# Performance work log

Measured on AMD Instinct MI355X. Metric: run time of the kernel, lower is better.

## Reference

```python
import jax, jax.numpy as jnp
import numpy as np

HALFKP = 64 * 5 * 64          # 20480
PAD = HALFKP                  # padding row index
L1, L2, L3 = 256, 31, 32
NB = 8                        # layer-stack / psqt buckets
EMB_DIM = L1 + NB             # 264


def setup_inputs() -> dict:
    key = jax.random.key(0)
    ks = jax.random.split(key, 16)
    B = 16384
    w_idx = jax.random.randint(ks[0], (B, 32), 0, HALFKP + 1)
    b_idx = jax.random.randint(ks[1], (B, 32), 0, HALFKP + 1)
    us = jax.random.uniform(ks[2], (B,), dtype=jnp.float32)
    them = jax.random.uniform(ks[3], (B,), dtype=jnp.float32)
    piece_count = jax.random.randint(ks[4], (B,), 2, 33)
    sigma = 0.025
    emb = jax.random.uniform(ks[5], (HALFKP + 1, EMB_DIM), jnp.float32, -sigma, sigma)
    emb = emb.at[PAD].set(0.0)
    def lin(k, out_f, in_f):
        bound = 1.0 / np.sqrt(in_f)
        k1, k2 = jax.random.split(k)
        W = jax.random.uniform(k1, (out_f, in_f), jnp.float32, -bound, bound)
        b = jax.random.uniform(k2, (out_f,), jnp.float32, -bound, bound)
        return W, b
    # StackedLinear init: replicate slot-0 weights across all buckets
    w1_0, b1_0 = lin(ks[6], L2 + 1, L1)
    w1 = jnp.tile(w1_0, (NB, 1)); b1 = jnp.tile(b1_0, NB)
    fw1 = jnp.zeros((L2 + 1, L1), jnp.float32)
    fb1 = jnp.zeros((L2 + 1,), jnp.float32)
    w2_0, b2_0 = lin(ks[7], L3, L2 * 2)
    w2 = jnp.tile(w2_0, (NB, 1)); b2 = jnp.tile(b2_0, NB)
    wo_0, _ = lin(ks[8], 1, L3)
    wo = jnp.tile(wo_0, (NB, 1)); bo = jnp.zeros((NB,), jnp.float32)
    return {"emb": emb, "w1": w1, "b1": b1, "fw1": fw1, "fb1": fb1,
            "w2": w2, "b2": b2, "wo": wo, "bo": bo,
            "us": us, "them": them,
            "w_idx": w_idx, "b_idx": b_idx, "piece_count": piece_count}


def reference(emb, w1, b1, fw1, fb1, w2, b2, wo, bo, us, them,
              w_idx, b_idx, piece_count):
    emb_eff = emb.at[PAD].set(0.0)                      # padding row contributes 0
    wp = emb_eff[w_idx].sum(axis=1)                     # [B, 264]
    bp = emb_eff[b_idx].sum(axis=1)
    w, wpsqt = wp[:, :L1], wp[:, L1:]
    b, bpsqt = bp[:, :L1], bp[:, L1:]
    us_c = us[:, None]; them_c = them[:, None]
    l0 = us_c * jnp.concatenate([w, b], 1) + them_c * jnp.concatenate([b, w], 1)
    l0 = jnp.clip(l0, 0.0, 1.0)                         # [B, 512]
    h = L1 // 2
    l0 = jnp.concatenate([l0[:, :h] * l0[:, h:2*h],
                          l0[:, 2*h:3*h] * l0[:, 3*h:]], 1) * (127.0 / 128.0)  # [B,256]
    bucket = jnp.clip((piece_count - 1) // 4, 0, 7)     # [B]
    # l1: factorized stacked linear, gather the bucket's slice only
    W1 = (w1 + jnp.tile(fw1, (NB, 1))).reshape(NB, L2 + 1, L1)
    B1 = (b1 + jnp.tile(fb1, NB)).reshape(NB, L2 + 1)
    l1c = jnp.einsum('bi,bji->bj', l0, W1[bucket]) + B1[bucket]   # [B,32]
    l1x, l1x_out = l1c[:, :L2], l1c[:, L2:]
    l1x = jnp.clip(jnp.concatenate([l1x * l1x * (255.0 / 256.0), l1x], 1), 0.0, 1.0)  # [B,62]
    W2 = w2.reshape(NB, L3, L2 * 2)
    l2x = jnp.clip(jnp.einsum('bi,bji->bj', l1x, W2[bucket]) + b2.reshape(NB, L3)[bucket], 0.0, 1.0)
    Wo = wo.reshape(NB, 1, L3)
    l3c = jnp.einsum('bi,bji->bj', l2x, Wo[bucket]) + bo.reshape(NB, 1)[bucket]       # [B,1]
    fc_out = l3c + l1x_out
    bk = bucket[:, None]
    psqt_out = (jnp.take_along_axis(wpsqt, bk, 1) - jnp.take_along_axis(bpsqt, bk, 1)) * (us_c - 0.5)
    return fc_out + psqt_out                            # [B,1]
```

## Files before the change

kernel.cpp:

```cpp
#include <hip/hip_runtime.h>

#define EMBD 264
#define NROWS 20481
#define NR4   5121
#define QS 5080.0f
#define INVQS (1.0f/5080.0f)

typedef short short8 __attribute__((ext_vector_type(8)));
typedef float f32x4  __attribute__((ext_vector_type(4)));

__device__ __forceinline__ float clamp01(float x) { return fminf(fmaxf(x, 0.f), 1.f); }
__device__ __forceinline__ unsigned short f2bf(float f) {
    unsigned u = __float_as_uint(f);
    u += 0x7fffu + ((u >> 16) & 1u);
    return (unsigned short)(u >> 16);
}

__global__ void prep_all(const float* __restrict__ emb, unsigned int* __restrict__ emb8,
                         float* __restrict__ psqt,
                         const float* __restrict__ w1, const float* __restrict__ fw1,
                         const float* __restrict__ b1, const float* __restrict__ fb1,
                         const float* __restrict__ w2,
                         unsigned short* __restrict__ w1b, float* __restrict__ b1c,
                         float* __restrict__ w2p) {
    if (blockIdx.x < NR4) {
        const int r = blockIdx.x * 4 + (threadIdx.x >> 6);
        const int t = threadIdx.x & 63;
        if (r >= NROWS) return;
        const bool pad = (r == NROWS - 1);
        const float4 v = *((const float4*)(emb + (size_t)r * EMBD) + t);
        int q0 = pad ? 128 : (int)rintf(v.x * QS) + 128;
        int q1 = pad ? 128 : (int)rintf(v.y * QS) + 128;
        int q2 = pad ? 128 : (int)rintf(v.z * QS) + 128;
        int q3 = pad ? 128 : (int)rintf(v.w * QS) + 128;
        q0 = min(max(q0, 0), 255); q1 = min(max(q1, 0), 255);
        q2 = min(max(q2, 0), 255); q3 = min(max(q3, 0), 255);
        emb8[(size_t)r * 64 + t] = (unsigned)q0 | ((unsigned)q1 << 8) |
                                   ((unsigned)q2 << 16) | ((unsigned)q3 << 24);
        if (t < 8) {
            float pv = emb[(size_t)r * EMBD + 256 + t];
            psqt[r * 8 + t] = pad ? 0.f : pv;
        }
    } else {
        const int e = (blockIdx.x - NR4) * 256 + threadIdx.x;
        const int bkt = e >> 13, rem = e & 8191;
        const int s = rem >> 10, rem2 = rem & 1023;
        const int nt = rem2 >> 9, rem3 = rem2 & 511;
        const int ln = rem3 >> 3, j = rem3 & 7;
        const int n  = nt * 16 + (ln & 15);
        const int hi = ln >> 4;
        const int k  = s * 32 + hi * 8 + j;
        const float v = w1[(bkt * 32 + n) * 256 + k] + fw1[n * 256 + k];
        w1b[e] = f2bf(v);
        if (e < 256) b1c[e] = b1[e] + fb1[e & 31];
        if (e < 16384) {
            const int jr = e >> 6, i = e & 63;
            float x = 0.f;
            if (i < 31) x = w2[jr * 62 + i];
            else if (i >= 32 && i < 63) x = w2[jr * 62 + i - 1];
            w2p[e] = x;
        }
    }
}

__global__ __launch_bounds__(256, 8) void g_phase1(
    const unsigned int* __restrict__ emb8,
    const float* __restrict__ psqt,
    const float* __restrict__ us,
    const float* __restrict__ them,
    const int*   __restrict__ w_idx,
    const int*   __restrict__ b_idx,
    const int*   __restrict__ pcnt,
    unsigned short* __restrict__ Ag,
    float* __restrict__ psq_g,
    int B)
{
    const int lane = threadIdx.x & 63;
    const int grow = __builtin_amdgcn_readfirstlane(blockIdx.x * 4 + (threadIdx.x >> 6));

    const float usv = us[grow];
    const float thv = them[grow];
    int bucket = (pcnt[grow] - 1) >> 2;
    bucket = bucket > 7 ? 7 : bucket;
    bucket = __builtin_amdgcn_readfirstlane(bucket);

    const int t = lane & 15;
    const int g = lane >> 4;
    const int d = (t << 2) + g;

    const int iv = (lane < 32) ? w_idx[grow * 32 + lane]
                               : b_idx[grow * 32 + (lane - 32)];

    float ps = psqt[(size_t)iv * 8 + bucket];

    uint4 vws[8], vbs[8];
#pragma unroll
    for (int k = 0; k < 8; ++k) {
        const int rw = __shfl(iv, (k << 2) + g);
        vws[k] = *(const uint4*)((const char*)emb8 +
                                 (((unsigned)rw << 8) + (unsigned)(t << 4)));
    }
#pragma unroll
    for (int k = 0; k < 8; ++k) {
        const int rb = __shfl(iv, 32 + (k << 2) + g);
        vbs[k] = *(const uint4*)((const char*)emb8 +
                                 (((unsigned)rb << 8) + (unsigned)(t << 4)));
    }

    const unsigned M = 0x00FF00FFu;
    unsigned a0w[4] = {0,0,0,0}, a1w[4] = {0,0,0,0};
    unsigned a0b[4] = {0,0,0,0}, a1b[4] = {0,0,0,0};
#pragma unroll
    for (int k = 0; k < 8; ++k) {
        a0w[0] += vws[k].x & M;  a1w[0] += (vws[k].x >> 8) & M;
        a0w[1] += vws[k].y & M;  a1w[1] += (vws[k].y >> 8) & M;
        a0w[2] += vws[k].z & M;  a1w[2] += (vws[k].z >> 8) & M;
        a0w[3] += vws[k].w & M;  a1w[3] += (vws[k].w >> 8) & M;
    }
#pragma unroll
    for (int k = 0; k < 8; ++k) {
        a0b[0] += vbs[k].x & M;  a1b[0] += (vbs[k].x >> 8) & M;
        a0b[1] += vbs[k].y & M;  a1b[1] += (vbs[k].y >> 8) & M;
        a0b[2] += vbs[k].z & M;  a1b[2] += (vbs[k].z >> 8) & M;
        a0b[3] += vbs[k].w & M;  a1b[3] += (vbs[k].w >> 8) & M;
    }

#pragma unroll
    for (int j = 0; j < 4; ++j) {
        a0w[j] += __shfl_xor(a0w[j], 16);  a0w[j] += __shfl_xor(a0w[j], 32);
        a1w[j] += __shfl_xor(a1w[j], 16);  a1w[j] += __shfl_xor(a1w[j], 32);
        a0b[j] += __shfl_xor(a0b[j], 16);  a0b[j] += __shfl_xor(a0b[j], 32);
        a1b[j] += __shfl_xor(a1b[j], 16);  a1b[j] += __shfl_xor(a1b[j], 32);
    }
    const bool gl = (g & 1) != 0, gh = (g & 2) != 0;
    const unsigned aw0 = gh ? (gl ? a0w[3] : a0w[2]) : (gl ? a0w[1] : a0w[0]);
    const unsigned aw1 = gh ? (gl ? a1w[3] : a1w[2]) : (gl ? a1w[1] : a1w[0]);
    const unsigned ab0 = gh ? (gl ? a0b[3] : a0b[2]) : (gl ? a0b[1] : a0b[0]);
    const unsigned ab1 = gh ? (gl ? a1b[3] : a1b[2]) : (gl ? a1b[1] : a1b[0]);

    ps += __shfl_xor(ps, 16);
    ps += __shfl_xor(ps, 8);
    ps += __shfl_xor(ps, 4);
    ps += __shfl_xor(ps, 2);
    ps += __shfl_xor(ps, 1);
    const float psq_w = __shfl(ps, 0);
    const float psq_b = __shfl(ps, 32);

    float4 aw4, ab4;
    aw4.x = ((int)(aw0 & 0xffffu) - 4096) * INVQS;
    aw4.y = ((int)(aw1 & 0xffffu) - 4096) * INVQS;
    aw4.z = ((int)(aw0 >> 16)     - 4096) * INVQS;
    aw4.w = ((int)(aw1 >> 16)     - 4096) * INVQS;
    ab4.x = ((int)(ab0 & 0xffffu) - 4096) * INVQS;
    ab4.y = ((int)(ab1 & 0xffffu) - 4096) * INVQS;
    ab4.z = ((int)(ab0 >> 16)     - 4096) * INVQS;
    ab4.w = ((int)(ab1 >> 16)     - 4096) * INVQS;

    float4 p, q;
    p.x = clamp01(usv * aw4.x + thv * ab4.x);
    p.y = clamp01(usv * aw4.y + thv * ab4.y);
    p.z = clamp01(usv * aw4.z + thv * ab4.z);
    p.w = clamp01(usv * aw4.w + thv * ab4.w);
    q.x = clamp01(usv * ab4.x + thv * aw4.x);
    q.y = clamp01(usv * ab4.y + thv * aw4.y);
    q.z = clamp01(usv * ab4.z + thv * aw4.z);
    q.w = clamp01(usv * ab4.w + thv * aw4.w);

    float4 po, qo;
    po.x = __shfl_xor(p.x, 8); po.y = __shfl_xor(p.y, 8);
    po.z = __shfl_xor(p.z, 8); po.w = __shfl_xor(p.w, 8);
    qo.x = __shfl_xor(q.x, 8); qo.y = __shfl_xor(q.y, 8);
    qo.z = __shfl_xor(q.z, 8); qo.w = __shfl_xor(q.w, 8);
    const float c127 = 127.f / 128.f;
    float4 l0f;
    if (t < 8) {
        l0f.x = p.x * po.x * c127; l0f.y = p.y * po.y * c127;
        l0f.z = p.z * po.z * c127; l0f.w = p.w * po.w * c127;
    } else {
        l0f.x = q.x * qo.x * c127; l0f.y = q.y * qo.y * c127;
        l0f.z = q.z * qo.z * c127; l0f.w = q.w * qo.w * c127;
    }

    const unsigned lo  = (unsigned)f2bf(l0f.x) | ((unsigned)f2bf(l0f.y) << 16);
    const unsigned hi2 = (unsigned)f2bf(l0f.z) | ((unsigned)f2bf(l0f.w) << 16);
    *((unsigned long long*)(Ag + (size_t)grow * 256 + d * 4)) =
        ((unsigned long long)hi2 << 32) | (unsigned long long)lo;
    if (lane == 0) psq_g[grow] = (psq_w - psq_b) * (usv - 0.5f);
}

__global__ __launch_bounds__(512) void g_phase23(
    const unsigned short* __restrict__ Ag,
    const float* __restrict__ psq_g,
    const unsigned short* __restrict__ w1b,
    const float* __restrict__ b1c,
    const float* __restrict__ w2p,
    const float* __restrict__ b2,
    const float* __restrict__ wo,
    const float* __restrict__ bo,
    const int*   __restrict__ pcnt,
    float* __restrict__ out,
    int B)
{
    __shared__ unsigned short A_lds[16 * 280];
    __shared__ float l1c[8 * 16 * 36];
    __shared__ float psq_lds[16];
    __shared__ int   bkt_lds[16];

    const int tid  = threadIdx.x;
    const int lane = tid & 63;
    const int w    = tid >> 6;

    {
        const int m = tid >> 5, c = tid & 31;
        *(uint4*)&A_lds[m * 280 + c * 8] =
            *(const uint4*)(Ag + ((size_t)blockIdx.x * 16 + m) * 256 + c * 8);
    }
    if (tid < 16) {
        const int row = blockIdx.x * 16 + tid;
        int bucket = (pcnt[row] - 1) >> 2;
        bkt_lds[tid] = bucket > 7 ? 7 : bucket;
        psq_lds[tid] = psq_g[row];
    }
    __syncthreads();

    {
        const int col = lane & 15;
        const int hi  = lane >> 4;
        const int bkt = w;
        f32x4 acc[2];
        acc[0] = (f32x4){0.f, 0.f, 0.f, 0.f};
        acc[1] = (f32x4){0.f, 0.f, 0.f, 0.f};

#pragma unroll
        for (int s = 0; s < 8; ++s) {
            const short8 a = *((const short8*)&A_lds[col * 280 + s * 32 + hi * 8]);
#pragma unroll
            for (int nt = 0; nt < 2; ++nt) {
                const short8 bf = *((const short8*)&w1b[(((bkt * 8 + s) * 2 + nt) * 64 + lane) * 8]);
                acc[nt] = __builtin_amdgcn_mfma_f32_16x16x32_bf16(a, bf, acc[nt], 0, 0, 0);
            }
        }
#pragma unroll
        for (int nt = 0; nt < 2; ++nt) {
            const float bias = b1c[bkt * 32 + nt * 16 + col];
#pragma unroll
            for (int reg = 0; reg < 4; ++reg) {
                const int mr = hi * 4 + reg;
                l1c[(bkt * 16 + mr) * 36 + nt * 16 + col] = acc[nt][reg] + bias;
            }
        }
    }
    __syncthreads();

    if (tid < 256) {
        const int row = tid >> 4;
        const int jj  = tid & 15;
        const int bkt = bkt_lds[row];
        const float4* crow = (const float4*)&l1c[(bkt * 16 + row) * 36];
        float4 c4[8];
#pragma unroll
        for (int b5 = 0; b5 < 8; ++b5) c4[b5] = crow[b5];

        const float4* wr0 = (const float4*)&w2p[(bkt * 32 + jj) * 64];
        const float4* wr1 = (const float4*)&w2p[(bkt * 32 + jj + 16) * 64];
        float acc0 = 0.f, acc1 = 0.f;
        const float kq = 255.f / 256.f;
#pragma unroll
        for (int b5 = 0; b5 < 8; ++b5) {
            const float4 cv = c4[b5];
            float4 sq, ln;
            sq.x = clamp01(cv.x * cv.x * kq); ln.x = clamp01(cv.x);
            sq.y = clamp01(cv.y * cv.y * kq); ln.y = clamp01(cv.y);
            sq.z = clamp01(cv.z * cv.z * kq); ln.z = clamp01(cv.z);
            sq.w = clamp01(cv.w * cv.w * kq); ln.w = clamp01(cv.w);
            const float4 ws0 = wr0[b5], wl0 = wr0[8 + b5];
            const float4 ws1 = wr1[b5], wl1 = wr1[8 + b5];
            acc0 += sq.x * ws0.x + sq.y * ws0.y + sq.z * ws0.z + sq.w * ws0.w;
            acc0 += ln.x * wl0.x + ln.y * wl0.y + ln.z * wl0.z + ln.w * wl0.w;
            acc1 += sq.x * ws1.x + sq.y * ws1.y + sq.z * ws1.z + sq.w * ws1.w;
            acc1 += ln.x * wl1.x + ln.y * wl1.y + ln.z * wl1.z + ln.w * wl1.w;
        }
        const float t0 = clamp01(acc0 + b2[bkt * 32 + jj])      * wo[bkt * 32 + jj];
        const float t1 = clamp01(acc1 + b2[bkt * 32 + jj + 16]) * wo[bkt * 32 + jj + 16];
        float tsum = t0 + t1;
        tsum += __shfl_xor(tsum, 8);
        tsum += __shfl_xor(tsum, 4);
        tsum += __shfl_xor(tsum, 2);
        tsum += __shfl_xor(tsum, 1);
        if (jj == 0) {
            out[blockIdx.x * 16 + row] = tsum + bo[bkt] + c4[7].w + psq_lds[row];
        }
    }
}

__global__ __launch_bounds__(256) void nnue_fwd_f32(
    const float* __restrict__ emb,
    const float* __restrict__ w1e, const float* __restrict__ fw1,
    const float* __restrict__ b1e, const float* __restrict__ fb1,
    const float* __restrict__ w2,  const float* __restrict__ b2,
    const float* __restrict__ wo,  const float* __restrict__ bo,
    const float* __restrict__ us,  const float* __restrict__ them,
    const int* __restrict__ w_idx, const int* __restrict__ b_idx,
    const int* __restrict__ pcnt,  float* __restrict__ out, int B)
{
    const int lane = threadIdx.x & 63;
    const int row  = blockIdx.x * 4 + (threadIdx.x >> 6);
    if (row >= B) return;
    const float usv = us[row];
    const float thv = them[row];
    int bucket = (pcnt[row] - 1) >> 2;
    bucket = bucket > 7 ? 7 : bucket;
    bucket = __builtin_amdgcn_readfirstlane(bucket);
    const int kk = lane & 31;
    const int myidx = (lane < 32) ? w_idx[row * 32 + kk] : b_idx[row * 32 + kk];
    float ps = emb[(size_t)myidx * EMBD + 256 + bucket];
    ps += __shfl_xor(ps, 16); ps += __shfl_xor(ps, 8);
    ps += __shfl_xor(ps, 4);  ps += __shfl_xor(ps, 2); ps += __shfl_xor(ps, 1);
    const float psq_w = __shfl(ps, 0);
    const float psq_b = __shfl(ps, 32);
    float4 aw = make_float4(0,0,0,0), ab = make_float4(0,0,0,0);
#pragma unroll
    for (int k = 0; k < 32; ++k) {
        const int iw = __shfl(myidx, k);
        const int ib = __shfl(myidx, 32 + k);
        const float4 vw = *((const float4*)(emb + (size_t)iw * EMBD) + lane);
        const float4 vb = *((const float4*)(emb + (size_t)ib * EMBD) + lane);
        aw.x += vw.x; aw.y += vw.y; aw.z += vw.z; aw.w += vw.w;
        ab.x += vb.x; ab.y += vb.y; ab.z += vb.z; ab.w += vb.w;
    }
    float4 p, q;
    p.x = clamp01(usv*aw.x + thv*ab.x); p.y = clamp01(usv*aw.y + thv*ab.y);
    p.z = clamp01(usv*aw.z + thv*ab.z); p.w = clamp01(usv*aw.w + thv*ab.w);
    q.x = clamp01(usv*ab.x + thv*aw.x); q.y = clamp01(usv*ab.y + thv*aw.y);
    q.z = clamp01(usv*ab.z + thv*aw.z); q.w = clamp01(usv*ab.w + thv*aw.w);
    float4 po, qo;
    po.x = __shfl_xor(p.x,32); po.y = __shfl_xor(p.y,32);
    po.z = __shfl_xor(p.z,32); po.w = __shfl_xor(p.w,32);
    qo.x = __shfl_xor(q.x,32); qo.y = __shfl_xor(q.y,32);
    qo.z = __shfl_xor(q.z,32); qo.w = __shfl_xor(q.w,32);
    const float c127 = 127.f/128.f;
    float4 l0f;
    if (lane < 32) { l0f.x=p.x*po.x*c127; l0f.y=p.y*po.y*c127; l0f.z=p.z*po.z*c127; l0f.w=p.w*po.w*c127; }
    else           { l0f.x=q.x*qo.x*c127; l0f.y=q.y*qo.y*c127; l0f.z=q.z*qo.z*c127; l0f.w=q.w*qo.w*c127; }
    float part[32];
    const float4* w1p = (const float4*)(w1e + (size_t)bucket * 8192);
    const float4* f1p = (const float4*)fw1;
#pragma unroll
    for (int j = 0; j < 32; ++j) {
        float4 wv = w1p[j*64 + lane];
        float4 fv = f1p[j*64 + lane];
        wv.x+=fv.x; wv.y+=fv.y; wv.z+=fv.z; wv.w+=fv.w;
        part[j] = l0f.x*wv.x + l0f.y*wv.y + l0f.z*wv.z + l0f.w*wv.w;
    }
#pragma unroll
    for (int j = 0; j < 32; ++j) {
        float v = part[j];
        v += __shfl_xor(v,32); v += __shfl_xor(v,16); v += __shfl_xor(v,8);
        v += __shfl_xor(v,4);  v += __shfl_xor(v,2);  v += __shfl_xor(v,1);
        part[j] = v + b1e[bucket*32 + j] + fb1[j];
    }
    const float l1x_out = part[31];
    float acc2 = 0.f;
    if (lane < 32) {
        const float* w2r = w2 + (size_t)(bucket*32 + lane) * 62;
#pragma unroll
        for (int i = 0; i < 31; ++i) {
            const float a = part[i];
            acc2 += clamp01(a*a*(255.f/256.f)) * w2r[i];
            acc2 += clamp01(a) * w2r[31+i];
        }
        acc2 += b2[bucket*32 + lane];
        acc2 = clamp01(acc2) * wo[bucket*32 + lane];
    }
    acc2 += __shfl_xor(acc2,16); acc2 += __shfl_xor(acc2,8);
    acc2 += __shfl_xor(acc2,4);  acc2 += __shfl_xor(acc2,2); acc2 += __shfl_xor(acc2,1);
    if (lane == 0)
        out[row] = acc2 + bo[bucket] + l1x_out + (psq_w - psq_b) * (usv - 0.5f);
}

extern "C" void kernel_launch(void* const* d_in, const int* in_sizes, int n_in,
                              void* d_out, int out_size, void* d_ws, size_t ws_size,
                              hipStream_t stream) {
    const float* emb  = (const float*)d_in[0];
    const float* w1   = (const float*)d_in[1];
    const float* b1   = (const float*)d_in[2];
    const float* fw1  = (const float*)d_in[3];
    const float* fb1  = (const float*)d_in[4];
    const float* w2   = (const float*)d_in[5];
    const float* b2   = (const float*)d_in[6];
    const float* wo   = (const float*)d_in[7];
    const float* bo   = (const float*)d_in[8];
    const float* us   = (const float*)d_in[9];
    const float* them = (const float*)d_in[10];
    const int*   wi   = (const int*)d_in[11];
    const int*   bi   = (const int*)d_in[12];
    const int*   pc   = (const int*)d_in[13];
    float* out = (float*)d_out;

    const int B = in_sizes[9];

    const size_t emb8_bytes = (size_t)NROWS * 256;
    const size_t psqt_bytes = (size_t)NROWS * 8 * 4;
    const size_t w1b_bytes  = 65536 * 2;
    const size_t b1c_bytes  = 256 * 4;
    const size_t w2p_bytes  = 16384 * 4;
    const size_t Ag_bytes   = (size_t)B * 256 * 2;
    const size_t psq_bytes  = (size_t)B * 4;
    const size_t need = emb8_bytes + psqt_bytes + w1b_bytes + b1c_bytes +
                        w2p_bytes + Ag_bytes + psq_bytes;

    if (ws_size >= need && (B % 16) == 0) {
        char* p = (char*)d_ws;
        unsigned int*   emb8 = (unsigned int*)p;     p += emb8_bytes;
        float*          psqt = (float*)p;            p += psqt_bytes;
        unsigned short* w1b  = (unsigned short*)p;   p += w1b_bytes;
        float*          b1c  = (float*)p;            p += b1c_bytes;
        float*          w2p  = (float*)p;            p += w2p_bytes;
        unsigned short* Ag   = (unsigned short*)p;   p += Ag_bytes;
        float*          psq  = (float*)p;

        prep_all<<<NR4 + 256, 256, 0, stream>>>(emb, emb8, psqt,
                                                w1, fw1, b1, fb1, w2, w1b, b1c, w2p);
        g_phase1<<<B / 4, 256, 0, stream>>>(emb8, psqt, us, them, wi, bi, pc,
                                            Ag, psq, B);
        g_phase23<<<B / 16, 512, 0, stream>>>(Ag, psq, w1b, b1c, w2p,
                                              b2, wo, bo, pc, out, B);
    } else {
        nnue_fwd_f32<<<(B + 3) / 4, 256, 0, stream>>>(emb, w1, fw1, b1, fb1,
                                                      w2, b2, wo, bo, us, them, wi, bi, pc, out, B);
    }
}
```

Before: 141.9 us.

## Tile phase1 gather by embedding column slice across blocks for cache locality

Restructures the embedding-gather kernel so each block handles one 32-byte column tile (of four) for 16 rows, with blocks interleaved so concurrently running blocks touch the same column slice of the embedding table. The aim is to shrink the active working set of the quantized embedding table and improve L2/MALL hit rates during the random row gathers. In exchange, indices and scalars are re-read once per tile, there are more cross-lane shuffle reductions, and PSQT is computed only by tile 0 blocks. The fast path now requires B divisible by 32.

```diff
diff --git a/kernel.cpp b/kernel.cpp
--- a/kernel.cpp
+++ b/kernel.cpp
@@ -63,7 +63,7 @@
     }
 }
 
-__global__ __launch_bounds__(256, 8) void g_phase1(
+__global__ __launch_bounds__(256, 8) void g_phase1t(
     const unsigned int* __restrict__ emb8,
     const float* __restrict__ psqt,
     const float* __restrict__ us,
@@ -75,117 +75,101 @@
     float* __restrict__ psq_g,
     int B)
 {
-    const int lane = threadIdx.x & 63;
-    const int grow = __builtin_amdgcn_readfirstlane(blockIdx.x * 4 + (threadIdx.x >> 6));
-
-    const float usv = us[grow];
-    const float thv = them[grow];
-    int bucket = (pcnt[grow] - 1) >> 2;
-    bucket = bucket > 7 ? 7 : bucket;
-    bucket = __builtin_amdgcn_readfirstlane(bucket);
-
-    const int t = lane & 15;
-    const int g = lane >> 4;
-    const int d = (t << 2) + g;
-
-    const int iv = (lane < 32) ? w_idx[grow * 32 + lane]
-                               : b_idx[grow * 32 + (lane - 32)];
-
-    float ps = psqt[(size_t)iv * 8 + bucket];
-
-    uint4 vws[8], vbs[8];
-#pragma unroll
-    for (int k = 0; k < 8; ++k) {
-        const int rw = __shfl(iv, (k << 2) + g);
-        vws[k] = *(const uint4*)((const char*)emb8 +
-                                 (((unsigned)rw << 8) + (unsigned)(t << 4)));
-    }
-#pragma unroll
-    for (int k = 0; k < 8; ++k) {
-        const int rb = __shfl(iv, 32 + (k << 2) + g);
-        vbs[k] = *(const uint4*)((const char*)emb8 +
-                                 (((unsigned)rb << 8) + (unsigned)(t << 4)));
-    }
-
+    const int bid   = blockIdx.x;
+    const int tile  = (bid & 7) >> 1;
+    const int chunk = ((bid >> 3) << 1) | (bid & 1);
+    const int c0    = tile << 5;
+
+    const int lane  = threadIdx.x & 63;
+    const int wv    = threadIdx.x >> 6;
+    const int slot  = lane >> 2;
+    const int piece = lane & 3;
+    const unsigned off = (unsigned)(c0 + ((piece & 1) << 4) + ((piece >> 1) << 7));
     const unsigned M = 0x00FF00FFu;
-    unsigned a0w[4] = {0,0,0,0}, a1w[4] = {0,0,0,0};
-    unsigned a0b[4] = {0,0,0,0}, a1b[4] = {0,0,0,0};
-#pragma unroll
-    for (int k = 0; k < 8; ++k) {
-        a0w[0] += vws[k].x & M;  a1w[0] += (vws[k].x >> 8) & M;
-        a0w[1] += vws[k].y & M;  a1w[1] += (vws[k].y >> 8) & M;
-        a0w[2] += vws[k].z & M;  a1w[2] += (vws[k].z >> 8) & M;
-        a0w[3] += vws[k].w & M;  a1w[3] += (vws[k].w >> 8) & M;
-    }
-#pragma unroll
-    for (int k = 0; k < 8; ++k) {
-        a0b[0] += vbs[k].x & M;  a1b[0] += (vbs[k].x >> 8) & M;
-        a0b[1] += vbs[k].y & M;  a1b[1] += (vbs[k].y >> 8) & M;
-        a0b[2] += vbs[k].z & M;  a1b[2] += (vbs[k].z >> 8) & M;
-        a0b[3] += vbs[k].w & M;  a1b[3] += (vbs[k].w >> 8) & M;
-    }
-
-#pragma unroll
-    for (int j = 0; j < 4; ++j) {
-        a0w[j] += __shfl_xor(a0w[j], 16);  a0w[j] += __shfl_xor(a0w[j], 32);
-        a1w[j] += __shfl_xor(a1w[j], 16);  a1w[j] += __shfl_xor(a1w[j], 32);
-        a0b[j] += __shfl_xor(a0b[j], 16);  a0b[j] += __shfl_xor(a0b[j], 32);
-        a1b[j] += __shfl_xor(a1b[j], 16);  a1b[j] += __shfl_xor(a1b[j], 32);
-    }
-    const bool gl = (g & 1) != 0, gh = (g & 2) != 0;
-    const unsigned aw0 = gh ? (gl ? a0w[3] : a0w[2]) : (gl ? a0w[1] : a0w[0]);
-    const unsigned aw1 = gh ? (gl ? a1w[3] : a1w[2]) : (gl ? a1w[1] : a1w[0]);
-    const unsigned ab0 = gh ? (gl ? a0b[3] : a0b[2]) : (gl ? a0b[1] : a0b[0]);
-    const unsigned ab1 = gh ? (gl ? a1b[3] : a1b[2]) : (gl ? a1b[1] : a1b[0]);
-
-    ps += __shfl_xor(ps, 16);
-    ps += __shfl_xor(ps, 8);
-    ps += __shfl_xor(ps, 4);
-    ps += __shfl_xor(ps, 2);
-    ps += __shfl_xor(ps, 1);
-    const float psq_w = __shfl(ps, 0);
-    const float psq_b = __shfl(ps, 32);
-
-    float4 aw4, ab4;
-    aw4.x = ((int)(aw0 & 0xffffu) - 4096) * INVQS;
-    aw4.y = ((int)(aw1 & 0xffffu) - 4096) * INVQS;
-    aw4.z = ((int)(aw0 >> 16)     - 4096) * INVQS;
-    aw4.w = ((int)(aw1 >> 16)     - 4096) * INVQS;
-    ab4.x = ((int)(ab0 & 0xffffu) - 4096) * INVQS;
-    ab4.y = ((int)(ab1 & 0xffffu) - 4096) * INVQS;
-    ab4.z = ((int)(ab0 >> 16)     - 4096) * INVQS;
-    ab4.w = ((int)(ab1 >> 16)     - 4096) * INVQS;
-
-    float4 p, q;
-    p.x = clamp01(usv * aw4.x + thv * ab4.x);
-    p.y = clamp01(usv * aw4.y + thv * ab4.y);
-    p.z = clamp01(usv * aw4.z + thv * ab4.z);
-    p.w = clamp01(usv * aw4.w + thv * ab4.w);
-    q.x = clamp01(usv * ab4.x + thv * aw4.x);
-    q.y = clamp01(usv * ab4.y + thv * aw4.y);
-    q.z = clamp01(usv * ab4.z + thv * aw4.z);
-    q.w = clamp01(usv * ab4.w + thv * aw4.w);
-
-    float4 po, qo;
-    po.x = __shfl_xor(p.x, 8); po.y = __shfl_xor(p.y, 8);
-    po.z = __shfl_xor(p.z, 8); po.w = __shfl_xor(p.w, 8);
-    qo.x = __shfl_xor(q.x, 8); qo.y = __shfl_xor(q.y, 8);
-    qo.z = __shfl_xor(q.z, 8); qo.w = __shfl_xor(q.w, 8);
     const float c127 = 127.f / 128.f;
-    float4 l0f;
-    if (t < 8) {
-        l0f.x = p.x * po.x * c127; l0f.y = p.y * po.y * c127;
-        l0f.z = p.z * po.z * c127; l0f.w = p.w * po.w * c127;
-    } else {
-        l0f.x = q.x * qo.x * c127; l0f.y = q.y * qo.y * c127;
-        l0f.z = q.z * qo.z * c127; l0f.w = q.w * qo.w * c127;
-    }
-
-    const unsigned lo  = (unsigned)f2bf(l0f.x) | ((unsigned)f2bf(l0f.y) << 16);
-    const unsigned hi2 = (unsigned)f2bf(l0f.z) | ((unsigned)f2bf(l0f.w) << 16);
-    *((unsigned long long*)(Ag + (size_t)grow * 256 + d * 4)) =
-        ((unsigned long long)hi2 << 32) | (unsigned long long)lo;
-    if (lane == 0) psq_g[grow] = (psq_w - psq_b) * (usv - 0.5f);
+
+    for (int rr = 0; rr < 4; ++rr) {
+        const int grow = __builtin_amdgcn_readfirstlane(chunk * 16 + wv * 4 + rr);
+        const float usv = us[grow];
+        const float thv = them[grow];
+
+        const int iv = (lane < 32) ? w_idx[grow * 32 + lane]
+                                   : b_idx[grow * 32 + (lane - 32)];
+
+        float ps = 0.f;
+        if (tile == 0) {
+            int bucket = (pcnt[grow] - 1) >> 2;
+            bucket = bucket > 7 ? 7 : bucket;
+            bucket = __builtin_amdgcn_readfirstlane(bucket);
+            ps = psqt[(size_t)iv * 8 + bucket];
+        }
+
+        unsigned aw[8] = {0,0,0,0,0,0,0,0}, ab[8] = {0,0,0,0,0,0,0,0};
+#pragma unroll
+        for (int k = 0; k < 2; ++k) {
+            const int r = __shfl(iv, k * 16 + slot);
+            const uint4 v = *(const uint4*)((const char*)emb8 +
+                                            (((unsigned)r << 8) + off));
+            aw[0] += v.x & M;  aw[1] += (v.x >> 8) & M;
+            aw[2] += v.y & M;  aw[3] += (v.y >> 8) & M;
+            aw[4] += v.z & M;  aw[5] += (v.z >> 8) & M;
+            aw[6] += v.w & M;  aw[7] += (v.w >> 8) & M;
+        }
+#pragma unroll
+        for (int k = 0; k < 2; ++k) {
+            const int r = __shfl(iv, 32 + k * 16 + slot);
+            const uint4 v = *(const uint4*)((const char*)emb8 +
+                                            (((unsigned)r << 8) + off));
+            ab[0] += v.x & M;  ab[1] += (v.x >> 8) & M;
+            ab[2] += v.y & M;  ab[3] += (v.y >> 8) & M;
+            ab[4] += v.z & M;  ab[5] += (v.z >> 8) & M;
+            ab[6] += v.w & M;  ab[7] += (v.w >> 8) & M;
+        }
+
+#pragma unroll
+        for (int i = 0; i < 8; ++i) {
+            aw[i] += __shfl_xor(aw[i], 4);   ab[i] += __shfl_xor(ab[i], 4);
+            aw[i] += __shfl_xor(aw[i], 8);   ab[i] += __shfl_xor(ab[i], 8);
+            aw[i] += __shfl_xor(aw[i], 16);  ab[i] += __shfl_xor(ab[i], 16);
+            aw[i] += __shfl_xor(aw[i], 32);  ab[i] += __shfl_xor(ab[i], 32);
+        }
+
+        if (tile == 0) {
+            ps += __shfl_xor(ps, 16);
+            ps += __shfl_xor(ps, 8);
+            ps += __shfl_xor(ps, 4);
+            ps += __shfl_xor(ps, 2);
+            ps += __shfl_xor(ps, 1);
+            const float psq_w = __shfl(ps, 0);
+            const float psq_b = __shfl(ps, 32);
+            if (lane == 0) psq_g[grow] = (psq_w - psq_b) * (usv - 0.5f);
+        }
+
+        unsigned outw[8];
+#pragma unroll
+        for (int c = 0; c < 16; c += 2) {
+            float o[2];
+#pragma unroll
+            for (int u = 0; u < 2; ++u) {
+                const int cc = c + u;
+                const int ai = ((cc >> 2) << 1) + (cc & 1);
+                const int sh = ((cc >> 1) & 1) << 4;
+                const float wv_ = ((int)((aw[ai] >> sh) & 0xffffu) - 4096) * INVQS;
+                const float bv_ = ((int)((ab[ai] >> sh) & 0xffffu) - 4096) * INVQS;
+                const float pv = clamp01(usv * wv_ + thv * bv_);
+                const float qv = clamp01(usv * bv_ + thv * wv_);
+                const float pp = __shfl_xor(pv, 2);
+                const float qp = __shfl_xor(qv, 2);
+                o[u] = (piece < 2) ? pv * pp * c127 : qv * qp * c127;
+            }
+            outw[c >> 1] = (unsigned)f2bf(o[0]) | ((unsigned)f2bf(o[1]) << 16);
+        }
+        if (slot == 0) {
+            unsigned short* dst = Ag + (size_t)grow * 256 + off;
+            *(uint4*)(dst)     = make_uint4(outw[0], outw[1], outw[2], outw[3]);
+            *(uint4*)(dst + 8) = make_uint4(outw[4], outw[5], outw[6], outw[7]);
+        }
+    }
 }
 
 __global__ __launch_bounds__(512) void g_phase23(
@@ -409,7 +393,7 @@
     const size_t need = emb8_bytes + psqt_bytes + w1b_bytes + b1c_bytes +
                         w2p_bytes + Ag_bytes + psq_bytes;
 
-    if (ws_size >= need && (B % 16) == 0) {
+    if (ws_size >= need && (B % 32) == 0) {
         char* p = (char*)d_ws;
         unsigned int*   emb8 = (unsigned int*)p;     p += emb8_bytes;
         float*          psqt = (float*)p;            p += psqt_bytes;
@@ -421,8 +405,8 @@
 
         prep_all<<<NR4 + 256, 256, 0, stream>>>(emb, emb8, psqt,
                                                 w1, fw1, b1, fb1, w2, w1b, b1c, w2p);
-        g_phase1<<<B / 4, 256, 0, stream>>>(emb8, psqt, us, them, wi, bi, pc,
-                                            Ag, psq, B);
+        g_phase1t<<<(B / 16) * 4, 256, 0, stream>>>(emb8, psqt, us, them, wi, bi, pc,
+                                                    Ag, psq, B);
         g_phase23<<<B / 16, 512, 0, stream>>>(Ag, psq, w1b, b1c, w2p,
                                               b2, wo, bo, pc, out, B);
     } else {
```

New measurement: 254.2 us. +79.1%, slower.
